# Kernel optimization log

Hardware: AMD Instinct MI355X
Metric: run time of the kernel (lower is better)

The kernel has to match this reference:

```python
import jax, jax.numpy as jnp
import numpy as np

W = 512
L = 512
M = 64  # number of target boxes

_CORNER_TEMPLATE = jnp.array(
    [[1, 1, -1], [1, -1, -1], [-1, -1, -1], [-1, 1, -1],
     [1, 1, 1], [1, -1, 1], [-1, -1, 1], [-1, 1, 1]], dtype=jnp.float32) * 0.5


def boxes_to_corners_3d_hwl(boxes):
    # boxes: (N, 7) = [x, y, z, h, w, l, yaw]; reorder dims to (l, w, h)
    dims = boxes[:, jnp.array([5, 4, 3])]
    corners = dims[:, None, :] * _CORNER_TEMPLATE  # (N, 8, 3)
    yaw = boxes[:, 6]
    c, s = jnp.cos(yaw), jnp.sin(yaw)
    z = jnp.zeros_like(c)
    o = jnp.ones_like(c)
    # rotate_points_along_z convention: points @ [[c, s, 0], [-s, c, 0], [0, 0, 1]]
    rot = jnp.stack([c, s, z, -s, c, z, z, z, o], axis=-1).reshape(-1, 3, 3)
    corners = jnp.einsum('nkc,ncd->nkd', corners, rot) + boxes[:, None, :3]
    return corners  # (N, 8, 3)


def corner_to_standup_2d(corners):
    # corners: (N, 8, 3) -> (N, 4) = [x1, y1, x2, y2]
    return jnp.stack([corners[..., 0].min(axis=1), corners[..., 1].min(axis=1),
                      corners[..., 0].max(axis=1), corners[..., 1].max(axis=1)], axis=-1)


def iou2d_batch(pred_boxes, target):
    # pred_boxes: (A, >=4), target: (M, 4) -> (A, M)
    bb_gt = target[None, :, :]      # (1, M, 4)
    bb_test = pred_boxes[:, None, :]  # (A, 1, 4)
    xx1 = jnp.maximum(bb_test[..., 0], bb_gt[..., 0])
    yy1 = jnp.maximum(bb_test[..., 1], bb_gt[..., 1])
    xx2 = jnp.minimum(bb_test[..., 2], bb_gt[..., 2])
    yy2 = jnp.minimum(bb_test[..., 3], bb_gt[..., 3])
    w = jnp.maximum(0.0, xx2 - xx1)
    h = jnp.maximum(0.0, yy2 - yy1)
    wh = w * h
    area_t = (bb_test[..., 2] - bb_test[..., 0]) * (bb_test[..., 3] - bb_test[..., 1])
    area_g = (bb_gt[..., 2] - bb_gt[..., 0]) * (bb_gt[..., 3] - bb_gt[..., 1])
    return wh / (area_t + area_g - wh)


def setup_inputs() -> dict:
    key = jax.random.key(0)
    k1, k2, k3, k4 = jax.random.split(key, 4)
    psm = jax.random.normal(k1, (1, 2, W, L), dtype=jnp.float32)
    rm = jax.random.normal(k2, (1, 14, W, L), dtype=jnp.float32) * 0.1
    # realistic anchor grid over a 100m x 100m BEV range, 2 yaw anchors per cell
    xs = jnp.linspace(0.0, 100.0, W, dtype=jnp.float32)
    ys = jnp.linspace(0.0, 100.0, L, dtype=jnp.float32)
    gx, gy = jnp.meshgrid(xs, ys, indexing='ij')  # (W, L)
    cz = jnp.full((W, L), -1.0, dtype=jnp.float32)
    h = jnp.full((W, L), 1.56, dtype=jnp.float32)
    ww = jnp.full((W, L), 1.6, dtype=jnp.float32)
    ll = jnp.full((W, L), 3.9, dtype=jnp.float32)
    base = jnp.stack([gx, gy, cz, h, ww, ll, jnp.zeros_like(gx)], axis=-1)  # (W, L, 7)
    a0 = base
    a1 = base.at[..., 6].set(jnp.float32(np.pi / 2))
    anchor_box = jnp.stack([a0, a1], axis=2)  # (W, L, 2, 7)
    # rigid transform: rotation about z by 0.3 rad + translation
    ang = 0.3
    T = np.eye(4, dtype=np.float32)
    T[0, 0] = np.cos(ang); T[0, 1] = -np.sin(ang)
    T[1, 0] = np.sin(ang); T[1, 1] = np.cos(ang)
    T[:3, 3] = [2.0, -1.5, 0.2]
    transformation_matrix = jnp.asarray(T)
    # M target boxes in hwl order
    u = jax.random.uniform(k3, (M, 7), dtype=jnp.float32)
    target = jnp.stack([
        u[:, 0] * 100.0, u[:, 1] * 100.0, -1.0 + 0.2 * u[:, 2],
        1.4 + 0.4 * u[:, 3], 1.5 + 0.4 * u[:, 4], 3.5 + 1.0 * u[:, 5],
        (u[:, 6] - 0.5) * jnp.float32(np.pi)], axis=-1)
    return {"psm": psm, "rm": rm, "anchor_box": anchor_box,
            "transformation_matrix": transformation_matrix, "target": target}


def reference(psm, rm, anchor_box, transformation_matrix, target):
    # --- convert_to_bbox_score ---
    prob = jax.nn.sigmoid(jnp.transpose(psm, (0, 2, 3, 1))).reshape(-1)  # (A,)
    deltas = jnp.transpose(rm, (0, 2, 3, 1)).reshape(-1, 7)              # (A, 7)
    anchors = anchor_box.reshape(-1, 7).astype(jnp.float32)              # (A, 7)
    anchors_d = jnp.sqrt(anchors[:, 4] ** 2 + anchors[:, 5] ** 2)
    xy = deltas[:, :2] * anchors_d[:, None] + anchors[:, :2]
    z = deltas[:, 2:3] * anchors[:, 3:4] + anchors[:, 2:3]
    dims = jnp.exp(deltas[:, 3:6]) * anchors[:, 3:6]
    yaw = (deltas[:, 6] + anchors[:, 6])[:, None]
    boxes3d = jnp.concatenate([xy, z, dims, yaw], axis=1)  # (A, 7)
    mask = (prob > 0.1).astype(prob.dtype)  # replaces masked_select (jit-static shapes)
    corners = boxes_to_corners_3d_hwl(boxes3d)  # (A, 8, 3)
    hom = jnp.concatenate([corners, jnp.ones(corners.shape[:2] + (1,), corners.dtype)], axis=-1)
    proj = jnp.einsum('nkc,oc->nko', hom, transformation_matrix)[..., :3]
    pred2d = corner_to_standup_2d(proj)  # (A, 4)
    # --- target boxes ---
    tgt_corners = boxes_to_corners_3d_hwl(target)
    tgt2d = corner_to_standup_2d(tgt_corners)  # (M, 4)
    # --- loss: sum_i log(1 - s_i) * sum_j IoU(pred_i, tgt_j), over masked preds ---
    ious = iou2d_batch(pred2d, tgt2d)  # (A, M)
    logs = jnp.log(1.0 - prob)
    loss = jnp.sum(mask * logs * jnp.sum(ious, axis=1))
    return loss
```

## Files before the change

### kernel.cpp

```cpp
#include <hip/hip_runtime.h>
#include <math.h>

#define WDIM 512
#define LDIM 512
#define MTGT 64
#define NCELL (WDIM * LDIM)

__global__ __launch_bounds__(256) void targeted_loss_kernel(
    const float* __restrict__ psm,
    const float* __restrict__ rm,
    const float* __restrict__ tmat,
    const float* __restrict__ target,
    float* __restrict__ out)
{
    __shared__ float s_t[MTGT * 5];
    __shared__ float s_part[4];

    const int tid = threadIdx.x;

    if (tid < MTGT) {
        const float tx  = target[tid * 7 + 0];
        const float ty  = target[tid * 7 + 1];
        const float tw  = target[tid * 7 + 4];
        const float tl  = target[tid * 7 + 5];
        const float tyaw = target[tid * 7 + 6];
        float sn, cs;
        sincosf(tyaw, &sn, &cs);
        const float ex = fabsf(cs) * (tl * 0.5f) + fabsf(sn) * (tw * 0.5f);
        const float ey = fabsf(sn) * (tl * 0.5f) + fabsf(cs) * (tw * 0.5f);
        const float x1 = tx - ex, y1 = ty - ey, x2 = tx + ex, y2 = ty + ey;
        s_t[tid * 5 + 0] = x1;
        s_t[tid * 5 + 1] = y1;
        s_t[tid * 5 + 2] = x2;
        s_t[tid * 5 + 3] = y2;
        s_t[tid * 5 + 4] = (x2 - x1) * (y2 - y1);
    }
    __syncthreads();

    const float T00 = tmat[0], T01 = tmat[1], T02 = tmat[2], T03 = tmat[3];
    const float T10 = tmat[4], T11 = tmat[5], T12 = tmat[6], T13 = tmat[7];

    const int cell = blockIdx.x * 256 + tid;

    float acc = 0.0f;
    {
        const int i = cell >> 9;
        const int j = cell & (LDIM - 1);
        const float step = 100.0f / 511.0f;
        const float gx = (float)i * step;
        const float gy = (float)j * step;
        const float ad = sqrtf(1.6f * 1.6f + 3.9f * 3.9f);

        float dch[14];
#pragma unroll
        for (int c = 0; c < 14; ++c) dch[c] = rm[c * NCELL + cell];
        const float plogit[2] = { psm[cell], psm[NCELL + cell] };

#pragma unroll
        for (int a = 0; a < 2; ++a) {
            const float* d = dch + a * 7;
            const float prob = 1.0f / (1.0f + expf(-plogit[a]));

            const float bx = fmaf(d[0], ad, gx);
            const float by = fmaf(d[1], ad, gy);
            const float bz = fmaf(d[2], 1.56f, -1.0f);
            const float bh = expf(d[3]) * 1.56f;
            const float bw = expf(d[4]) * 1.6f;
            const float bl = expf(d[5]) * 3.9f;
            const float yaw = d[6] + (a ? 1.57079632679489662f : 0.0f);

            float sn, cs;
            sincosf(yaw, &sn, &cs);

            const float pcx = T03 + T00 * bx + T01 * by + T02 * bz;
            const float pcy = T13 + T10 * bx + T11 * by + T12 * bz;
            const float A0 = T00 * cs + T01 * sn, B0 = T01 * cs - T00 * sn;
            const float A1 = T10 * cs + T11 * sn, B1 = T11 * cs - T10 * sn;
            const float ex = fabsf(A0) * (bl * 0.5f) + fabsf(B0) * (bw * 0.5f)
                           + fabsf(T02) * (bh * 0.5f);
            const float ey = fabsf(A1) * (bl * 0.5f) + fabsf(B1) * (bw * 0.5f)
                           + fabsf(T12) * (bh * 0.5f);

            const float x1 = pcx - ex, y1 = pcy - ey;
            const float x2 = pcx + ex, y2 = pcy + ey;
            const float areaP = (x2 - x1) * (y2 - y1);

            float isum = 0.0f;
#pragma unroll 8
            for (int m = 0; m < MTGT; ++m) {
                const float tx1 = s_t[m * 5 + 0];
                const float ty1 = s_t[m * 5 + 1];
                const float tx2 = s_t[m * 5 + 2];
                const float ty2 = s_t[m * 5 + 3];
                const float ag  = s_t[m * 5 + 4];
                float ww = fminf(x2, tx2) - fmaxf(x1, tx1);
                float hh = fminf(y2, ty2) - fmaxf(y1, ty1);
                ww = fmaxf(ww, 0.0f);
                hh = fmaxf(hh, 0.0f);
                const float wh = ww * hh;
                isum += wh * __builtin_amdgcn_rcpf(areaP + ag - wh);
            }
            if (prob > 0.1f) acc += logf(1.0f - prob) * isum;
        }
    }

#pragma unroll
    for (int off = 32; off > 0; off >>= 1) acc += __shfl_down(acc, off, 64);
    if ((tid & 63) == 0) s_part[tid >> 6] = acc;
    __syncthreads();
    if (tid == 0) {
        atomicAdd(out, s_part[0] + s_part[1] + s_part[2] + s_part[3]);
    }
}

extern "C" void kernel_launch(void* const* d_in, const int* in_sizes, int n_in,
                              void* d_out, int out_size, void* d_ws, size_t ws_size,
                              hipStream_t stream) {
    const float* psm    = (const float*)d_in[0];
    const float* rm     = (const float*)d_in[1];
    const float* tmat   = (const float*)d_in[3];
    const float* target = (const float*)d_in[4];
    float* out = (float*)d_out;

    hipMemsetAsync(out, 0, sizeof(float), stream);

    const int blocks = NCELL / 256;
    targeted_loss_kernel<<<blocks, 256, 0, stream>>>(psm, rm, tmat, target, out);
}
```

Measured before the change: 99.12 us.

## Cull targets per block via bounding-box test and use 2D block tiles

Result: faster. 93.93 us (-5.2%).

```diff
diff --git a/kernel.cpp b/kernel.cpp
--- a/kernel.cpp
+++ b/kernel.cpp
@@ -6,6 +6,9 @@
 #define MTGT 64
 #define NCELL (WDIM * LDIM)
 
+#define TI 4
+#define TJ 64
+
 __global__ __launch_bounds__(256) void targeted_loss_kernel(
     const float* __restrict__ psm,
     const float* __restrict__ rm,
@@ -13,104 +16,130 @@
     const float* __restrict__ target,
     float* __restrict__ out)
 {
-    __shared__ float s_t[MTGT * 5];
-    __shared__ float s_part[4];
+    __shared__ float4 s_t[MTGT];
+    __shared__ float4 s_list[MTGT];
+    __shared__ float  s_red[16];
+    __shared__ int    s_cnt;
+    __shared__ float  s_part[4];
 
-    const int tid = threadIdx.x;
+    const int tid  = threadIdx.x;
+    const int lane = tid & 63;
+    const int wv   = tid >> 6;
+
+    const float T00 = tmat[0], T01 = tmat[1], T02 = tmat[2], T03 = tmat[3];
+    const float T10 = tmat[4], T11 = tmat[5], T12 = tmat[6], T13 = tmat[7];
 
     if (tid < MTGT) {
         const float tx  = target[tid * 7 + 0];
         const float ty  = target[tid * 7 + 1];
         const float tw  = target[tid * 7 + 4];
         const float tl  = target[tid * 7 + 5];
-        const float tyaw = target[tid * 7 + 6];
-        float sn, cs;
-        sincosf(tyaw, &sn, &cs);
+        const float tyw = target[tid * 7 + 6];
+        const float sn = __sinf(tyw), cs = __cosf(tyw);
         const float ex = fabsf(cs) * (tl * 0.5f) + fabsf(sn) * (tw * 0.5f);
         const float ey = fabsf(sn) * (tl * 0.5f) + fabsf(cs) * (tw * 0.5f);
-        const float x1 = tx - ex, y1 = ty - ey, x2 = tx + ex, y2 = ty + ey;
-        s_t[tid * 5 + 0] = x1;
-        s_t[tid * 5 + 1] = y1;
-        s_t[tid * 5 + 2] = x2;
-        s_t[tid * 5 + 3] = y2;
-        s_t[tid * 5 + 4] = (x2 - x1) * (y2 - y1);
+        s_t[tid] = make_float4(tx - ex, ty - ey, tx + ex, ty + ey);
+    }
+
+    const int bi = blockIdx.x >> 3;
+    const int bj = blockIdx.x & 7;
+    const int i  = bi * TI + wv;
+    const int j  = bj * TJ + lane;
+    const int cell = i * LDIM + j;
+
+    const float step = 100.0f / 511.0f;
+    const float gx = (float)i * step;
+    const float gy = (float)j * step;
+    const float ad = 4.21556879f;
+
+    float dch[14];
+#pragma unroll
+    for (int c = 0; c < 14; ++c) dch[c] = rm[c * NCELL + cell];
+    const float pl[2] = { psm[cell], psm[NCELL + cell] };
+
+    float X1[2], Y1[2], X2[2], Y2[2], AP[2], LG[2];
+#pragma unroll
+    for (int a = 0; a < 2; ++a) {
+        const float* d = dch + a * 7;
+        const float bx = fmaf(d[0], ad, gx);
+        const float by = fmaf(d[1], ad, gy);
+        const float bz = fmaf(d[2], 1.56f, -1.0f);
+        const float bh = __expf(d[3]) * 1.56f;
+        const float bw = __expf(d[4]) * 1.6f;
+        const float bl = __expf(d[5]) * 3.9f;
+        const float yaw = d[6] + (a ? 1.57079632679489662f : 0.0f);
+        const float sn = __sinf(yaw), cs = __cosf(yaw);
+        const float pcx = T03 + T00 * bx + T01 * by + T02 * bz;
+        const float pcy = T13 + T10 * bx + T11 * by + T12 * bz;
+        const float A0 = T00 * cs + T01 * sn, B0 = T01 * cs - T00 * sn;
+        const float A1 = T10 * cs + T11 * sn, B1 = T11 * cs - T10 * sn;
+        const float ex = fabsf(A0) * (bl * 0.5f) + fabsf(B0) * (bw * 0.5f)
+                       + fabsf(T02) * (bh * 0.5f);
+        const float ey = fabsf(A1) * (bl * 0.5f) + fabsf(B1) * (bw * 0.5f)
+                       + fabsf(T12) * (bh * 0.5f);
+        X1[a] = pcx - ex; Y1[a] = pcy - ey;
+        X2[a] = pcx + ex; Y2[a] = pcy + ey;
+        AP[a] = (X2[a] - X1[a]) * (Y2[a] - Y1[a]);
+        const float lg = -__logf(1.0f + __expf(pl[a]));
+        LG[a] = (pl[a] > -2.1972246f) ? lg : 0.0f;
+    }
+
+    float mnx = fminf(X1[0], X1[1]), mny = fminf(Y1[0], Y1[1]);
+    float mxx = fmaxf(X2[0], X2[1]), mxy = fmaxf(Y2[0], Y2[1]);
+#pragma unroll
+    for (int o = 32; o > 0; o >>= 1) {
+        mnx = fminf(mnx, __shfl_xor(mnx, o, 64));
+        mny = fminf(mny, __shfl_xor(mny, o, 64));
+        mxx = fmaxf(mxx, __shfl_xor(mxx, o, 64));
+        mxy = fmaxf(mxy, __shfl_xor(mxy, o, 64));
+    }
+    if (lane == 0) {
+        s_red[wv * 4 + 0] = mnx; s_red[wv * 4 + 1] = mny;
+        s_red[wv * 4 + 2] = mxx; s_red[wv * 4 + 3] = mxy;
     }
     __syncthreads();
 
-    const float T00 = tmat[0], T01 = tmat[1], T02 = tmat[2], T03 = tmat[3];
-    const float T10 = tmat[4], T11 = tmat[5], T12 = tmat[6], T13 = tmat[7];
+    if (tid < 64) {
+        const float bx1 = fminf(fminf(s_red[0], s_red[4]),  fminf(s_red[8],  s_red[12]));
+        const float by1 = fminf(fminf(s_red[1], s_red[5]),  fminf(s_red[9],  s_red[13]));
+        const float bx2 = fmaxf(fmaxf(s_red[2], s_red[6]),  fmaxf(s_red[10], s_red[14]));
+        const float by2 = fmaxf(fmaxf(s_red[3], s_red[7]),  fmaxf(s_red[11], s_red[15]));
+        const float4 t = s_t[tid];
+        const bool hit = (t.x <= bx2) && (t.z >= bx1) && (t.y <= by2) && (t.w >= by1);
+        const unsigned long long msk = __ballot(hit);
+        if (hit) {
+            const int pos = __popcll(msk & ((1ull << lane) - 1ull));
+            s_list[pos] = t;
+        }
+        if (lane == 0) s_cnt = (int)__popcll(msk);
+    }
+    __syncthreads();
 
-    const int cell = blockIdx.x * 256 + tid;
-
-    float acc = 0.0f;
-    {
-        const int i = cell >> 9;
-        const int j = cell & (LDIM - 1);
-        const float step = 100.0f / 511.0f;
-        const float gx = (float)i * step;
-        const float gy = (float)j * step;
-        const float ad = sqrtf(1.6f * 1.6f + 3.9f * 3.9f);
-
-        float dch[14];
-#pragma unroll
-        for (int c = 0; c < 14; ++c) dch[c] = rm[c * NCELL + cell];
-        const float plogit[2] = { psm[cell], psm[NCELL + cell] };
+    const int cnt = s_cnt;
+    float is0 = 0.0f, is1 = 0.0f;
+    for (int m = 0; m < cnt; ++m) {
+        const float4 t = s_list[m];
+        const float ag = (t.z - t.x) * (t.w - t.y);
+        {
+            const float ww = fmaxf(fminf(X2[0], t.z) - fmaxf(X1[0], t.x), 0.0f);
+            const float hh = fmaxf(fminf(Y2[0], t.w) - fmaxf(Y1[0], t.y), 0.0f);
+            const float wh = ww * hh;
+            is0 += wh * __builtin_amdgcn_rcpf(AP[0] + ag - wh);
+        }
+        {
+            const float ww = fmaxf(fminf(X2[1], t.z) - fmaxf(X1[1], t.x), 0.0f);
+            const float hh = fmaxf(fminf(Y2[1], t.w) - fmaxf(Y1[1], t.y), 0.0f);
+            const float wh = ww * hh;
+            is1 += wh * __builtin_amdgcn_rcpf(AP[1] + ag - wh);
+        }
+    }
+    float acc = LG[0] * is0 + LG[1] * is1;
 
 #pragma unroll
-        for (int a = 0; a < 2; ++a) {
-            const float* d = dch + a * 7;
-            const float prob = 1.0f / (1.0f + expf(-plogit[a]));
-
-            const float bx = fmaf(d[0], ad, gx);
-            const float by = fmaf(d[1], ad, gy);
-            const float bz = fmaf(d[2], 1.56f, -1.0f);
-            const float bh = expf(d[3]) * 1.56f;
-            const float bw = expf(d[4]) * 1.6f;
-            const float bl = expf(d[5]) * 3.9f;
-            const float yaw = d[6] + (a ? 1.57079632679489662f : 0.0f);
-
-            float sn, cs;
-            sincosf(yaw, &sn, &cs);
-
-            const float pcx = T03 + T00 * bx + T01 * by + T02 * bz;
-            const float pcy = T13 + T10 * bx + T11 * by + T12 * bz;
-            const float A0 = T00 * cs + T01 * sn, B0 = T01 * cs - T00 * sn;
-            const float A1 = T10 * cs + T11 * sn, B1 = T11 * cs - T10 * sn;
-            const float ex = fabsf(A0) * (bl * 0.5f) + fabsf(B0) * (bw * 0.5f)
-                           + fabsf(T02) * (bh * 0.5f);
-            const float ey = fabsf(A1) * (bl * 0.5f) + fabsf(B1) * (bw * 0.5f)
-                           + fabsf(T12) * (bh * 0.5f);
-
-            const float x1 = pcx - ex, y1 = pcy - ey;
-            const float x2 = pcx + ex, y2 = pcy + ey;
-            const float areaP = (x2 - x1) * (y2 - y1);
-
-            float isum = 0.0f;
-#pragma unroll 8
-            for (int m = 0; m < MTGT; ++m) {
-                const float tx1 = s_t[m * 5 + 0];
-                const float ty1 = s_t[m * 5 + 1];
-                const float tx2 = s_t[m * 5 + 2];
-                const float ty2 = s_t[m * 5 + 3];
-                const float ag  = s_t[m * 5 + 4];
-                float ww = fminf(x2, tx2) - fmaxf(x1, tx1);
-                float hh = fminf(y2, ty2) - fmaxf(y1, ty1);
-                ww = fmaxf(ww, 0.0f);
-                hh = fmaxf(hh, 0.0f);
-                const float wh = ww * hh;
-                isum += wh * __builtin_amdgcn_rcpf(areaP + ag - wh);
-            }
-            if (prob > 0.1f) acc += logf(1.0f - prob) * isum;
-        }
-    }
-
-#pragma unroll
-    for (int off = 32; off > 0; off >>= 1) acc += __shfl_down(acc, off, 64);
-    if ((tid & 63) == 0) s_part[tid >> 6] = acc;
+    for (int o = 32; o > 0; o >>= 1) acc += __shfl_down(acc, o, 64);
+    if (lane == 0) s_part[wv] = acc;
     __syncthreads();
-    if (tid == 0) {
-        atomicAdd(out, s_part[0] + s_part[1] + s_part[2] + s_part[3]);
-    }
+    if (tid == 0) atomicAdd(out, s_part[0] + s_part[1] + s_part[2] + s_part[3]);
 }
 
 extern "C" void kernel_launch(void* const* d_in, const int* in_sizes, int n_in,
@@ -124,6 +153,6 @@
 
     hipMemsetAsync(out, 0, sizeof(float), stream);
 
-    const int blocks = NCELL / 256;
+    const int blocks = (WDIM / TI) * (LDIM / TJ);
     targeted_loss_kernel<<<blocks, 256, 0, stream>>>(psm, rm, tmat, target, out);
 }
```
